# Performance work log

Hardware: AMD Instinct MI355X
Metric: run time of the kernel (lower is better)

Reference implementation:

```python
import jax, jax.numpy as jnp
import numpy as np

B, OBS, D, V = 32, 768, 512, 64  # batch, obs_dim, latent/action/embed dim, max_vars


def _gelu(x):
    return jax.nn.gelu(x, approximate=False)  # torch nn.GELU default is exact erf


def setup_inputs() -> dict:
    key = jax.random.key(0)
    ks = jax.random.split(key, 16)
    s = lambda k, shape, scale=0.02: (jax.random.normal(k, shape, jnp.float32) * scale)
    return {
        "obs": jax.random.normal(ks[0], (B, OBS), jnp.float32),
        "action": jax.random.normal(ks[1], (B, D), jnp.float32),
        # CausalGraphLearner params
        "embed": jax.random.normal(ks[2], (V, D), jnp.float32),  # nn.Embedding weight
        "sc_w1": s(ks[3], (2 * D, 3 * D)), "sc_b1": jnp.zeros((2 * D,), jnp.float32),
        "sc_w2": s(ks[4], (1, 2 * D)), "sc_b2": jnp.zeros((1,), jnp.float32),
        # WorldModelEngine params
        "enc_w1": s(ks[5], (2 * D, OBS)), "enc_b1": jnp.zeros((2 * D,), jnp.float32),
        "enc_w2": s(ks[6], (D, 2 * D)), "enc_b2": jnp.zeros((D,), jnp.float32),
        "gru_wih": s(ks[7], (3 * D, 2 * D)), "gru_whh": s(ks[8], (3 * D, D)),
        "gru_bih": jnp.zeros((3 * D,), jnp.float32), "gru_bhh": jnp.zeros((3 * D,), jnp.float32),
        "dec_w": s(ks[9], (OBS, D)), "dec_b": jnp.zeros((OBS,), jnp.float32),
        # reasoner params
        "rs_w1": s(ks[10], (D, D)), "rs_b1": jnp.zeros((D,), jnp.float32),
        "rs_w2": s(ks[11], (D, D)), "rs_b2": jnp.zeros((D,), jnp.float32),
    }


def reference(obs, action, embed, sc_w1, sc_b1, sc_w2, sc_b2,
              enc_w1, enc_b1, enc_w2, enc_b2,
              gru_wih, gru_whh, gru_bih, gru_bhh,
              dec_w, dec_b, rs_w1, rs_b1, rs_w2, rs_b2):
    # --- WorldModelEngine ---
    z = _gelu(obs @ enc_w1.T + enc_b1) @ enc_w2.T + enc_b2            # [B, D]
    x = jnp.concatenate([z, action], axis=-1)                          # [B, 2D]
    h0 = jnp.zeros((obs.shape[0], D), obs.dtype)                       # h=None -> zeros
    gi = x @ gru_wih.T + gru_bih                                       # [B, 3D]
    gh = h0 @ gru_whh.T + gru_bhh                                      # [B, 3D]
    r = jax.nn.sigmoid(gi[:, :D] + gh[:, :D])
    u = jax.nn.sigmoid(gi[:, D:2 * D] + gh[:, D:2 * D])
    n = jnp.tanh(gi[:, 2 * D:] + r * gh[:, 2 * D:])
    h = (1.0 - u) * n + u * h0                                         # [B, D]
    pred = h @ dec_w.T + dec_b                                         # [B, OBS]

    # --- CausalGraphLearner ---
    # Linear-of-concat identity: W1 @ cat(cause, effect, ctx) = Wa@cause + Wb@effect + Wc@ctx
    Wa, Wb, Wc = sc_w1[:, :D], sc_w1[:, D:2 * D], sc_w1[:, 2 * D:]
    Ea = embed @ Wa.T                                                  # [V, 2D]
    Eb = embed @ Wb.T                                                  # [V, 2D]
    Cc = (h + action) @ Wc.T                                           # [B, 2D]
    hid = _gelu(Cc[:, None, None, :] + Ea[None, :, None, :]
                + Eb[None, None, :, :] + sc_b1)                        # [B, V, V, 2D]
    scores = jax.nn.sigmoid(jnp.einsum('bijd,d->bij', hid, sc_w2[0]) + sc_b2[0])  # [B,V,V]
    graph = scores.mean(0)                                             # [V, V] (returned scores)

    # --- reasoner ---
    reasoning = _gelu(h @ rs_w1.T + rs_b1) @ rs_w2.T + rs_b2           # [B, D]

    return (h, pred, graph, reasoning)
```

## Files before the change

kernel.cpp:

```cpp
#include <hip/hip_runtime.h>
#include <math.h>


#if __has_builtin(__builtin_amdgcn_exp2f)
#define EXP2F __builtin_amdgcn_exp2f
#else
#define EXP2F exp2f
#endif

__device__ __forceinline__ float gelu_exact(float x) {
    return 0.5f * x * (1.f + erff(x * 0.70710678118654752f));
}
__device__ __forceinline__ float sigmoid_fast(float v) {
    return __builtin_amdgcn_rcpf(1.f + EXP2F(-1.442695041f * v));
}
__device__ __forceinline__ float tanh_fast(float v) {
    return fmaf(-2.f, __builtin_amdgcn_rcpf(1.f + EXP2F(2.885390082f * v)), 1.f);
}

template<int NF4, int ACT, int BT>
__device__ __forceinline__ void wgemm(int wid,
        const float* __restrict__ A, int lda,
        const float* __restrict__ W, int ldw,
        const float* __restrict__ bias,
        float* __restrict__ out, int ldo,
        int oblocks) {
    int lane = threadIdx.x & 63;
    int oblock = wid % oblocks;
    int bgroup = wid / oblocks;
    int o0 = oblock * 8, b0 = bgroup * BT;

    float4 w[8][NF4];
#pragma unroll
    for (int r = 0; r < 8; ++r) {
        const float4* wr = reinterpret_cast<const float4*>(W + (o0 + r) * ldw);
#pragma unroll
        for (int c = 0; c < NF4; ++c) w[r][c] = wr[c * 64 + lane];
    }
    float bv = bias ? bias[o0 + (lane & 7)] : 0.f;
    bool p0 = lane & 1, p1 = lane & 2, p2 = lane & 4;

#pragma unroll
    for (int bi = 0; bi < BT; ++bi) {
        const float4* ar = reinterpret_cast<const float4*>(A + (b0 + bi) * lda);
        float4 a[NF4];
#pragma unroll
        for (int c = 0; c < NF4; ++c) a[c] = ar[c * 64 + lane];
        float s[8];
#pragma unroll
        for (int r = 0; r < 8; ++r) {
            float acc = 0.f;
#pragma unroll
            for (int c = 0; c < NF4; ++c) {
                acc = fmaf(a[c].x, w[r][c].x, acc);
                acc = fmaf(a[c].y, w[r][c].y, acc);
                acc = fmaf(a[c].z, w[r][c].z, acc);
                acc = fmaf(a[c].w, w[r][c].w, acc);
            }
            s[r] = acc;
        }
        float m[4];
#pragma unroll
        for (int k = 0; k < 4; ++k) {
            float keep = p0 ? s[2 * k + 1] : s[2 * k];
            float send = p0 ? s[2 * k] : s[2 * k + 1];
            m[k] = keep + __shfl_xor(send, 1, 64);
        }
        float n[2];
#pragma unroll
        for (int k = 0; k < 2; ++k) {
            float keep = p1 ? m[2 * k + 1] : m[2 * k];
            float send = p1 ? m[2 * k] : m[2 * k + 1];
            n[k] = keep + __shfl_xor(send, 2, 64);
        }
        float F;
        {
            float keep = p2 ? n[1] : n[0];
            float send = p2 ? n[0] : n[1];
            F = keep + __shfl_xor(send, 4, 64);
        }
        F += __shfl_xor(F, 8, 64);
        F += __shfl_xor(F, 16, 64);
        F += __shfl_xor(F, 32, 64);
        float v = F + bv;
        if (ACT) v = gelu_exact(v);
        if (lane < 8) out[(b0 + bi) * ldo + o0 + lane] = v;
    }
}

__global__ void __launch_bounds__(256) front_kernel(
    const float* __restrict__ obs, const float* __restrict__ enc_w1,
    const float* __restrict__ enc_b1, float* __restrict__ h1,
    const float* __restrict__ embed, const float* __restrict__ sc_w1,
    const float* __restrict__ sc_b1, float* __restrict__ Ea, float* __restrict__ Eb,
    const float* __restrict__ action, const float* __restrict__ wih,
    const float* __restrict__ bih, float* __restrict__ gia) {
    int wid = blockIdx.x * 4 + (threadIdx.x >> 6);
    if (wid < 512) {
        wgemm<3, 1, 8>(wid, obs, 768, enc_w1, 768, enc_b1, h1, 1024, 128);
    } else if (wid < 1536) {
        wgemm<2, 0, 8>(wid - 512, embed, 512, sc_w1, 1536, sc_b1, Ea, 1024, 128);
    } else if (wid < 2560) {
        wgemm<2, 0, 8>(wid - 1536, embed, 512, sc_w1 + 512, 1536, nullptr, Eb, 1024, 128);
    } else {
        wgemm<2, 0, 8>(wid - 2560, action, 512, wih + 512, 1024, bih, gia, 1536, 192);
    }
}

__global__ void __launch_bounds__(256) enc2_kernel(
    const float* __restrict__ h1, const float* __restrict__ enc_w2,
    const float* __restrict__ enc_b2, float* __restrict__ z) {
    int wid = blockIdx.x * 4 + (threadIdx.x >> 6);
    wgemm<4, 0, 2>(wid, h1, 1024, enc_w2, 1024, enc_b2, z, 512, 64);
}

__global__ void __launch_bounds__(256) gigru_kernel(
    const float* __restrict__ z, const float* __restrict__ wih,
    const float* __restrict__ gia, const float* __restrict__ bhh,
    const float* __restrict__ action, float* __restrict__ h, float* __restrict__ ha) {
    int wid = blockIdx.x * 4 + (threadIdx.x >> 6);
    int lane = threadIdx.x & 63;
    int opair = wid & 255;
    int bg = wid >> 8;
    int o0 = opair * 2, b0 = bg * 2;

    int rows[6] = {o0, o0 + 1, 512 + o0, 513 + o0, 1024 + o0, 1025 + o0};
    float4 w[6][2];
#pragma unroll
    for (int r = 0; r < 6; ++r) {
        const float4* wr = reinterpret_cast<const float4*>(wih + rows[r] * 1024);
#pragma unroll
        for (int c = 0; c < 2; ++c) w[r][c] = wr[c * 64 + lane];
    }
    float bhr0 = bhh[o0],        bhr1 = bhh[o0 + 1];
    float bhu0 = bhh[512 + o0],  bhu1 = bhh[513 + o0];
    float bhn0 = bhh[1024 + o0], bhn1 = bhh[1025 + o0];

#pragma unroll
    for (int bi = 0; bi < 2; ++bi) {
        int b = b0 + bi;
        const float4* ar = reinterpret_cast<const float4*>(z + b * 512);
        float4 a[2] = {ar[lane], ar[64 + lane]};
        float s[6];
#pragma unroll
        for (int r = 0; r < 6; ++r) {
            float acc = 0.f;
#pragma unroll
            for (int c = 0; c < 2; ++c) {
                acc = fmaf(a[c].x, w[r][c].x, acc);
                acc = fmaf(a[c].y, w[r][c].y, acc);
                acc = fmaf(a[c].z, w[r][c].z, acc);
                acc = fmaf(a[c].w, w[r][c].w, acc);
            }
            s[r] = acc;
        }
#pragma unroll
        for (int m = 1; m < 64; m <<= 1) {
#pragma unroll
            for (int r = 0; r < 6; ++r) s[r] += __shfl_xor(s[r], m, 64);
        }
        if (lane == 0) {
            const float* gb = gia + b * 1536;
            float r0 = sigmoid_fast(s[0] + gb[o0]        + bhr0);
            float r1 = sigmoid_fast(s[1] + gb[o0 + 1]    + bhr1);
            float u0 = sigmoid_fast(s[2] + gb[512 + o0]  + bhu0);
            float u1 = sigmoid_fast(s[3] + gb[513 + o0]  + bhu1);
            float n0 = tanh_fast(s[4] + gb[1024 + o0] + r0 * bhn0);
            float n1 = tanh_fast(s[5] + gb[1025 + o0] + r1 * bhn1);
            float hv0 = (1.f - u0) * n0;
            float hv1 = (1.f - u1) * n1;
            h[b * 512 + o0]      = hv0;
            h[b * 512 + o0 + 1]  = hv1;
            ha[b * 512 + o0]     = hv0 + action[b * 512 + o0];
            ha[b * 512 + o0 + 1] = hv1 + action[b * 512 + o0 + 1];
        }
    }
}

__global__ void __launch_bounds__(256) mid_kernel(
    const float* __restrict__ h, const float* __restrict__ ha,
    const float* __restrict__ dec_w, const float* __restrict__ dec_b, float* __restrict__ pred,
    const float* __restrict__ rs_w1, const float* __restrict__ rs_b1, float* __restrict__ r1,
    const float* __restrict__ sc_w1, float* __restrict__ Cc) {
    int wid = blockIdx.x * 4 + (threadIdx.x >> 6);
    if (wid < 1536) {
        wgemm<2, 0, 2>(wid, h, 512, dec_w, 512, dec_b, pred, 768, 96);
    } else if (wid < 2560) {
        wgemm<2, 1, 2>(wid - 1536, h, 512, rs_w1, 512, rs_b1, r1, 512, 64);
    } else {
        wgemm<2, 0, 2>(wid - 2560, ha, 512, sc_w1 + 1024, 1536, nullptr, Cc, 1024, 128);
    }
}

__global__ void __launch_bounds__(256) score_rs2_kernel(
    const float* __restrict__ Ea, const float* __restrict__ Eb,
    const float* __restrict__ Cc, const float* __restrict__ w2,
    const float* __restrict__ b2, float* __restrict__ graph,
    const float* __restrict__ r1, const float* __restrict__ rs_w2,
    const float* __restrict__ rs_b2, float* __restrict__ reasoning) {
    int blk = blockIdx.x;
    if (blk < 64) {
        int wid = blk * 4 + (threadIdx.x >> 6);
        wgemm<2, 0, 8>(wid, r1, 512, rs_w2, 512, rs_b2, reasoning, 512, 64);
    }
    int i = blk >> 5;
    int j0 = (blk & 31) << 1;
    int lane = threadIdx.x & 63;
    int wave = threadIdx.x >> 6;
    int d0 = lane << 4;

    const float4* Ea4  = reinterpret_cast<const float4*>(Ea + i * 1024 + d0);
    const float4* Eb04 = reinterpret_cast<const float4*>(Eb + j0 * 1024 + d0);
    const float4* Eb14 = reinterpret_cast<const float4*>(Eb + (j0 + 1) * 1024 + d0);
    const float4* W4   = reinterpret_cast<const float4*>(w2 + d0);

    float basea[16], baseb[16], wv[16];
#pragma unroll
    for (int c = 0; c < 4; ++c) {
        float4 e  = Ea4[c];
        float4 f0 = Eb04[c];
        float4 f1 = Eb14[c];
        float4 w  = W4[c];
        basea[4 * c + 0] = e.x + f0.x; basea[4 * c + 1] = e.y + f0.y;
        basea[4 * c + 2] = e.z + f0.z; basea[4 * c + 3] = e.w + f0.w;
        baseb[4 * c + 0] = e.x + f1.x; baseb[4 * c + 1] = e.y + f1.y;
        baseb[4 * c + 2] = e.z + f1.z; baseb[4 * c + 3] = e.w + f1.w;
        wv[4 * c + 0] = w.x; wv[4 * c + 1] = w.y;
        wv[4 * c + 2] = w.z; wv[4 * c + 3] = w.w;
    }

    const float NK = -2.4554274f;
    float sA[8], sB[8];
#pragma unroll
    for (int b = 0; b < 8; ++b) { sA[b] = 0.f; sB[b] = 0.f; }

    const float* ccbase = Cc + (wave * 8) * 1024 + d0;
#pragma unroll
    for (int b = 0; b < 8; ++b) {
        const float4* q = reinterpret_cast<const float4*>(ccbase + b * 1024);
        float4 c0 = q[0], c1 = q[1], c2 = q[2], c3 = q[3];
        float cc[16] = {c0.x, c0.y, c0.z, c0.w, c1.x, c1.y, c1.z, c1.w,
                        c2.x, c2.y, c2.z, c2.w, c3.x, c3.y, c3.z, c3.w};
#pragma unroll
        for (int e = 0; e < 16; e += 2) {
            float xa0 = cc[e] + basea[e];
            float xa1 = cc[e + 1] + basea[e + 1];
            float ta0 = EXP2F(xa0 * NK);
            float ta1 = EXP2F(xa1 * NK);
            float da0 = 1.f + ta0, da1 = 1.f + ta1;
            float numa = fmaf(xa0 * wv[e], da1, (xa1 * wv[e + 1]) * da0);
            sA[b] = fmaf(numa, __builtin_amdgcn_rcpf(da0 * da1), sA[b]);

            float xb0 = cc[e] + baseb[e];
            float xb1 = cc[e + 1] + baseb[e + 1];
            float tb0 = EXP2F(xb0 * NK);
            float tb1 = EXP2F(xb1 * NK);
            float db0 = 1.f + tb0, db1 = 1.f + tb1;
            float numb = fmaf(xb0 * wv[e], db1, (xb1 * wv[e + 1]) * db0);
            sB[b] = fmaf(numb, __builtin_amdgcn_rcpf(db0 * db1), sB[b]);
        }
    }

    bool p0 = lane & 1, p1 = lane & 2, p2 = lane & 4, p3 = lane & 8;
    float m[8];
#pragma unroll
    for (int k = 0; k < 8; ++k) {
        float keep = p0 ? sB[k] : sA[k];
        float send = p0 ? sA[k] : sB[k];
        m[k] = keep + __shfl_xor(send, 1, 64);
    }
    float n[4];
#pragma unroll
    for (int k = 0; k < 4; ++k) {
        float keep = p1 ? m[2 * k + 1] : m[2 * k];
        float send = p1 ? m[2 * k] : m[2 * k + 1];
        n[k] = keep + __shfl_xor(send, 2, 64);
    }
    float o2[2];
#pragma unroll
    for (int k = 0; k < 2; ++k) {
        float keep = p2 ? n[2 * k + 1] : n[2 * k];
        float send = p2 ? n[2 * k] : n[2 * k + 1];
        o2[k] = keep + __shfl_xor(send, 4, 64);
    }
    float F;
    {
        float keep = p3 ? o2[1] : o2[0];
        float send = p3 ? o2[0] : o2[1];
        F = keep + __shfl_xor(send, 8, 64);
    }
    F += __shfl_xor(F, 16, 64);
    F += __shfl_xor(F, 32, 64);

    float sig = sigmoid_fast(F + b2[0]);
    sig += __shfl_xor(sig, 2, 64);
    sig += __shfl_xor(sig, 4, 64);
    sig += __shfl_xor(sig, 8, 64);

    __shared__ float red[4][2];
    if (lane < 2) red[wave][lane] = sig;
    __syncthreads();
    if (threadIdx.x < 2) {
        graph[i * 64 + j0 + threadIdx.x] =
            (red[0][threadIdx.x] + red[1][threadIdx.x] +
             red[2][threadIdx.x] + red[3][threadIdx.x]) * 0.03125f;
    }
}

extern "C" void kernel_launch(void* const* d_in, const int* in_sizes, int n_in,
                              void* d_out, int out_size, void* d_ws, size_t ws_size,
                              hipStream_t stream) {
    const float* obs     = (const float*)d_in[0];
    const float* action  = (const float*)d_in[1];
    const float* embed   = (const float*)d_in[2];
    const float* sc_w1   = (const float*)d_in[3];
    const float* sc_b1   = (const float*)d_in[4];
    const float* sc_w2   = (const float*)d_in[5];
    const float* sc_b2   = (const float*)d_in[6];
    const float* enc_w1  = (const float*)d_in[7];
    const float* enc_b1  = (const float*)d_in[8];
    const float* enc_w2  = (const float*)d_in[9];
    const float* enc_b2  = (const float*)d_in[10];
    const float* gru_wih = (const float*)d_in[11];
    const float* gru_bih = (const float*)d_in[13];
    const float* gru_bhh = (const float*)d_in[14];
    const float* dec_w   = (const float*)d_in[15];
    const float* dec_b   = (const float*)d_in[16];
    const float* rs_w1   = (const float*)d_in[17];
    const float* rs_b1   = (const float*)d_in[18];
    const float* rs_w2   = (const float*)d_in[19];
    const float* rs_b2   = (const float*)d_in[20];

    float* ws = (float*)d_ws;
    float* h1  = ws + 0;
    float* z   = ws + 32768;
    float* gia = ws + 49152;
    float* ha  = ws + 98304;
    float* r1  = ws + 114688;
    float* Cc  = ws + 131072;
    float* Ea  = ws + 163840;
    float* Eb  = ws + 229376;

    float* h_out     = (float*)d_out;
    float* pred      = h_out + 16384;
    float* graph     = h_out + 40960;
    float* reasoning = h_out + 45056;

    front_kernel<<<832, 256, 0, stream>>>(obs, enc_w1, enc_b1, h1,
                                          embed, sc_w1, sc_b1, Ea, Eb,
                                          action, gru_wih, gru_bih, gia);
    enc2_kernel<<<256, 256, 0, stream>>>(h1, enc_w2, enc_b2, z);
    gigru_kernel<<<1024, 256, 0, stream>>>(z, gru_wih, gia, gru_bhh, action, h_out, ha);
    mid_kernel<<<1152, 256, 0, stream>>>(h_out, ha, dec_w, dec_b, pred,
                                         rs_w1, rs_b1, r1, sc_w1, Cc);
    score_rs2_kernel<<<2048, 256, 0, stream>>>(Ea, Eb, Cc, sc_w2, sc_b2, graph,
                                               r1, rs_w2, rs_b2, reasoning);
}
```

Measured before the change: 172.8 us.

## Split score kernel across 8 waves per block and halve front GEMM batch tile

The score kernel now runs 512-thread blocks with 8 waves, each wave handling 4 batch rows instead of 8. The Cc values are preloaded into registers ahead of the compute loop, and the butterfly reduction is reworked to match. The front kernel's GEMMs use a batch tile of 4 instead of 8, which doubles the wave count and the grid size. The aim is more parallelism and better latency hiding in the two heaviest kernels, at the cost of reloading weights for more batch groups and a larger cross-wave shared-memory reduction.

Result: slower. 188.8 us (+9.3%).

```diff
diff --git a/kernel.cpp b/kernel.cpp
--- a/kernel.cpp
+++ b/kernel.cpp
@@ -96,14 +96,14 @@
     const float* __restrict__ action, const float* __restrict__ wih,
     const float* __restrict__ bih, float* __restrict__ gia) {
     int wid = blockIdx.x * 4 + (threadIdx.x >> 6);
-    if (wid < 512) {
-        wgemm<3, 1, 8>(wid, obs, 768, enc_w1, 768, enc_b1, h1, 1024, 128);
-    } else if (wid < 1536) {
-        wgemm<2, 0, 8>(wid - 512, embed, 512, sc_w1, 1536, sc_b1, Ea, 1024, 128);
-    } else if (wid < 2560) {
-        wgemm<2, 0, 8>(wid - 1536, embed, 512, sc_w1 + 512, 1536, nullptr, Eb, 1024, 128);
+    if (wid < 1024) {
+        wgemm<3, 1, 4>(wid, obs, 768, enc_w1, 768, enc_b1, h1, 1024, 128);
+    } else if (wid < 3072) {
+        wgemm<2, 0, 4>(wid - 1024, embed, 512, sc_w1, 1536, sc_b1, Ea, 1024, 128);
+    } else if (wid < 5120) {
+        wgemm<2, 0, 4>(wid - 3072, embed, 512, sc_w1 + 512, 1536, nullptr, Eb, 1024, 128);
     } else {
-        wgemm<2, 0, 8>(wid - 2560, action, 512, wih + 512, 1024, bih, gia, 1536, 192);
+        wgemm<2, 0, 4>(wid - 5120, action, 512, wih + 512, 1024, bih, gia, 1536, 192);
     }
 }
 
@@ -192,21 +192,22 @@
     }
 }
 
-__global__ void __launch_bounds__(256) score_rs2_kernel(
+__global__ void __launch_bounds__(512) score_rs2_kernel(
     const float* __restrict__ Ea, const float* __restrict__ Eb,
     const float* __restrict__ Cc, const float* __restrict__ w2,
     const float* __restrict__ b2, float* __restrict__ graph,
     const float* __restrict__ r1, const float* __restrict__ rs_w2,
     const float* __restrict__ rs_b2, float* __restrict__ reasoning) {
     int blk = blockIdx.x;
-    if (blk < 64) {
-        int wid = blk * 4 + (threadIdx.x >> 6);
+    int tid = threadIdx.x;
+    int lane = tid & 63;
+    int wave = tid >> 6;
+    if (blk < 32) {
+        int wid = blk * 8 + wave;
         wgemm<2, 0, 8>(wid, r1, 512, rs_w2, 512, rs_b2, reasoning, 512, 64);
     }
     int i = blk >> 5;
     int j0 = (blk & 31) << 1;
-    int lane = threadIdx.x & 63;
-    int wave = threadIdx.x >> 6;
     int d0 = lane << 4;
 
     const float4* Ea4  = reinterpret_cast<const float4*>(Ea + i * 1024 + d0);
@@ -229,30 +230,40 @@
         wv[4 * c + 2] = w.z; wv[4 * c + 3] = w.w;
     }
 
+    float cc[4][16];
+    {
+        const float* ccbase = Cc + (wave * 4) * 1024 + d0;
+#pragma unroll
+        for (int r = 0; r < 4; ++r) {
+            const float4* q = reinterpret_cast<const float4*>(ccbase + r * 1024);
+            float4 c0 = q[0], c1 = q[1], c2 = q[2], c3 = q[3];
+            cc[r][0]  = c0.x; cc[r][1]  = c0.y; cc[r][2]  = c0.z; cc[r][3]  = c0.w;
+            cc[r][4]  = c1.x; cc[r][5]  = c1.y; cc[r][6]  = c1.z; cc[r][7]  = c1.w;
+            cc[r][8]  = c2.x; cc[r][9]  = c2.y; cc[r][10] = c2.z; cc[r][11] = c2.w;
+            cc[r][12] = c3.x; cc[r][13] = c3.y; cc[r][14] = c3.z; cc[r][15] = c3.w;
+        }
+    }
+
     const float NK = -2.4554274f;
-    float sA[8], sB[8];
-#pragma unroll
-    for (int b = 0; b < 8; ++b) { sA[b] = 0.f; sB[b] = 0.f; }
-
-    const float* ccbase = Cc + (wave * 8) * 1024 + d0;
-#pragma unroll
-    for (int b = 0; b < 8; ++b) {
-        const float4* q = reinterpret_cast<const float4*>(ccbase + b * 1024);
-        float4 c0 = q[0], c1 = q[1], c2 = q[2], c3 = q[3];
-        float cc[16] = {c0.x, c0.y, c0.z, c0.w, c1.x, c1.y, c1.z, c1.w,
-                        c2.x, c2.y, c2.z, c2.w, c3.x, c3.y, c3.z, c3.w};
+    float sA[4], sB[4];
+#pragma unroll
+    for (int b = 0; b < 4; ++b) { sA[b] = 0.f; sB[b] = 0.f; }
+
+#pragma unroll
+    for (int b = 0; b < 4; ++b) {
 #pragma unroll
         for (int e = 0; e < 16; e += 2) {
-            float xa0 = cc[e] + basea[e];
-            float xa1 = cc[e + 1] + basea[e + 1];
+            float c0 = cc[b][e], c1 = cc[b][e + 1];
+            float xa0 = c0 + basea[e];
+            float xa1 = c1 + basea[e + 1];
             float ta0 = EXP2F(xa0 * NK);
             float ta1 = EXP2F(xa1 * NK);
             float da0 = 1.f + ta0, da1 = 1.f + ta1;
             float numa = fmaf(xa0 * wv[e], da1, (xa1 * wv[e + 1]) * da0);
             sA[b] = fmaf(numa, __builtin_amdgcn_rcpf(da0 * da1), sA[b]);
 
-            float xb0 = cc[e] + baseb[e];
-            float xb1 = cc[e + 1] + baseb[e + 1];
+            float xb0 = c0 + baseb[e];
+            float xb1 = c1 + baseb[e + 1];
             float tb0 = EXP2F(xb0 * NK);
             float tb1 = EXP2F(xb1 * NK);
             float db0 = 1.f + tb0, db1 = 1.f + tb1;
@@ -261,49 +272,43 @@
         }
     }
 
-    bool p0 = lane & 1, p1 = lane & 2, p2 = lane & 4, p3 = lane & 8;
-    float m[8];
-#pragma unroll
-    for (int k = 0; k < 8; ++k) {
+    bool p0 = lane & 1, p1 = lane & 2, p2 = lane & 4;
+    float m[4];
+#pragma unroll
+    for (int k = 0; k < 4; ++k) {
         float keep = p0 ? sB[k] : sA[k];
         float send = p0 ? sA[k] : sB[k];
         m[k] = keep + __shfl_xor(send, 1, 64);
     }
-    float n[4];
-#pragma unroll
-    for (int k = 0; k < 4; ++k) {
+    float n[2];
+#pragma unroll
+    for (int k = 0; k < 2; ++k) {
         float keep = p1 ? m[2 * k + 1] : m[2 * k];
         float send = p1 ? m[2 * k] : m[2 * k + 1];
         n[k] = keep + __shfl_xor(send, 2, 64);
     }
-    float o2[2];
-#pragma unroll
-    for (int k = 0; k < 2; ++k) {
-        float keep = p2 ? n[2 * k + 1] : n[2 * k];
-        float send = p2 ? n[2 * k] : n[2 * k + 1];
-        o2[k] = keep + __shfl_xor(send, 4, 64);
-    }
     float F;
     {
-        float keep = p3 ? o2[1] : o2[0];
-        float send = p3 ? o2[0] : o2[1];
-        F = keep + __shfl_xor(send, 8, 64);
-    }
+        float keep = p2 ? n[1] : n[0];
+        float send = p2 ? n[0] : n[1];
+        F = keep + __shfl_xor(send, 4, 64);
+    }
+    F += __shfl_xor(F, 8, 64);
     F += __shfl_xor(F, 16, 64);
     F += __shfl_xor(F, 32, 64);
 
     float sig = sigmoid_fast(F + b2[0]);
     sig += __shfl_xor(sig, 2, 64);
     sig += __shfl_xor(sig, 4, 64);
-    sig += __shfl_xor(sig, 8, 64);
-
-    __shared__ float red[4][2];
+
+    __shared__ float red[8][2];
     if (lane < 2) red[wave][lane] = sig;
     __syncthreads();
-    if (threadIdx.x < 2) {
-        graph[i * 64 + j0 + threadIdx.x] =
-            (red[0][threadIdx.x] + red[1][threadIdx.x] +
-             red[2][threadIdx.x] + red[3][threadIdx.x]) * 0.03125f;
+    if (tid < 2) {
+        float g = 0.f;
+#pragma unroll
+        for (int wv8 = 0; wv8 < 8; ++wv8) g += red[wv8][tid];
+        graph[i * 64 + j0 + tid] = g * 0.03125f;
     }
 }
 
@@ -346,13 +351,13 @@
     float* graph     = h_out + 40960;
     float* reasoning = h_out + 45056;
 
-    front_kernel<<<832, 256, 0, stream>>>(obs, enc_w1, enc_b1, h1,
-                                          embed, sc_w1, sc_b1, Ea, Eb,
-                                          action, gru_wih, gru_bih, gia);
+    front_kernel<<<1664, 256, 0, stream>>>(obs, enc_w1, enc_b1, h1,
+                                           embed, sc_w1, sc_b1, Ea, Eb,
+                                           action, gru_wih, gru_bih, gia);
     enc2_kernel<<<256, 256, 0, stream>>>(h1, enc_w2, enc_b2, z);
     gigru_kernel<<<1024, 256, 0, stream>>>(z, gru_wih, gia, gru_bhh, action, h_out, ha);
     mid_kernel<<<1152, 256, 0, stream>>>(h_out, ha, dec_w, dec_b, pred,
                                          rs_w1, rs_b1, r1, sc_w1, Cc);
-    score_rs2_kernel<<<2048, 256, 0, stream>>>(Ea, Eb, Cc, sc_w2, sc_b2, graph,
+    score_rs2_kernel<<<2048, 512, 0, stream>>>(Ea, Eb, Cc, sc_w2, sc_b2, graph,
                                                r1, rs_w2, rs_b2, reasoning);
 }
```
